# Performance work log

Measured on AMD Instinct MI355X. Metric: run time of the kernel, lower is better.

## Reference

```python
import jax, jax.numpy as jnp
import numpy as np

D = 128          # embedding dim
N_INIT = 100000  # number of initial (axiom) clauses
L = 64           # topological levels of derived clauses
M = 4096         # derived clauses per level
N_THAX = 2000    # distinct axiom-name (thax) embeddings
N_SINE = 32      # sine-level embeddings
N_RULES = 256    # distinct inference rules (each with its own 2-ary MLP)
N_TOT = N_INIT + L * M


def setup_inputs() -> dict:
    key = jax.random.key(0)
    ks = jax.random.split(key, 10)
    rng = np.random.default_rng(0)
    # parents of level-l nodes point to any node created strictly earlier
    parents = np.stack(
        [rng.integers(0, N_INIT + l * M, size=(M, 2)) for l in range(L)]
    ).astype(np.int32)  # [L, M, 2]
    return {
        "thax_table": jax.random.normal(ks[0], (N_THAX, D), jnp.float32) * 0.1,
        "sine_table": jax.random.normal(ks[1], (N_SINE, D), jnp.float32) * 0.1,
        "rule_W": jax.random.normal(ks[2], (N_RULES, 2 * D, D), jnp.float32) * (1.0 / np.sqrt(2 * D)),
        "rule_b": jax.random.normal(ks[3], (N_RULES, D), jnp.float32) * 0.01,
        "eval_w": jax.random.normal(ks[4], (D,), jnp.float32) * (1.0 / np.sqrt(D)),
        "eval_b": jax.random.normal(ks[5], (1,), jnp.float32) * 0.01,
        "pos_vals": jax.random.uniform(ks[6], (N_TOT,), jnp.float32, 0.01, 1.0),
        "neg_vals": jax.random.uniform(ks[7], (N_TOT,), jnp.float32, 0.01, 1.0),
        "init_thax": jax.random.randint(ks[8], (N_INIT,), 0, N_THAX, jnp.int32),
        "init_sine": jax.random.randint(ks[9], (N_INIT,), 0, N_SINE, jnp.int32),
        "parents": jnp.asarray(parents),
        "rules": jnp.asarray(rng.integers(0, N_RULES, size=(L, M)).astype(np.int32)),
    }


def reference(thax_table, sine_table, rule_W, rule_b, eval_w, eval_b,
              pos_vals, neg_vals, init_thax, init_sine, parents, rules):
    n_init = init_thax.shape[0]
    n_lvl, m = rules.shape
    d = thax_table.shape[1]

    # init nodes: embed = init_embeds[thax]() + sine_embedder(sine)
    init_emb = thax_table[init_thax] + sine_table[init_sine]  # [N_INIT, D]
    store0 = jnp.concatenate(
        [init_emb, jnp.zeros((n_lvl * m, d), init_emb.dtype)], axis=0)  # [N_TOT, D]

    # deriv nodes, level by level: gather 2 parents, per-rule MLP (cat -> Linear -> ReLU)
    def step(store, xs):
        lvl, par, rul = xs                       # par: [M,2] int, rul: [M] int
        pe = store[par].reshape(m, 2 * d)        # gather parent embeddings
        emb = jax.nn.relu(jnp.einsum('mi,mio->mo', pe, rule_W[rul]) + rule_b[rul])
        store = jax.lax.dynamic_update_slice(store, emb, (n_init + lvl * m, 0))
        return store, None

    store, _ = jax.lax.scan(step, store0, (jnp.arange(n_lvl), parents, rules))

    # eval_net + weighted BCEWithLogits (pos_weight = tot_neg / tot_pos)
    logits = store @ eval_w + eval_b[0]          # [N_TOT]
    tot = pos_vals + neg_vals
    y = pos_vals / tot
    pw = jnp.sum(neg_vals) / jnp.sum(pos_vals)
    per_node = pw * y * jax.nn.softplus(-logits) + (1.0 - y) * jax.nn.softplus(logits)
    loss = jnp.sum(tot * per_node).reshape(1)
    posOK = jnp.sum(jnp.where(logits >= 0.0, pos_vals, 0.0))
    negOK = jnp.sum(jnp.where(logits < 0.0, neg_vals, 0.0))
    return (loss, posOK, negOK)
```

## Files before the change

kernel.cpp:

```cpp
#include <hip/hip_runtime.h>

#define D      128
#define NINIT  100000
#define LVLS   64
#define M      4096
#define NRULES 256
#define NTOT   (NINIT + LVLS * M)
#define NBLK   256
#define NTHR   512
#define GRID_THREADS (NBLK * NTHR)

typedef __attribute__((ext_vector_type(8))) short short8;
typedef __attribute__((ext_vector_type(4))) float floatx4;

#define ST_OFF 256
#define SI_OFF (ST_OFF + (size_t)NTOT * D * 2)
#define RO_OFF (SI_OFF + (size_t)LVLS * M * 4)
#define FL_OFF (RO_OFF + (size_t)LVLS * (NRULES + 1) * 4)

__device__ __forceinline__ unsigned short f2bf(float x) {
  unsigned u = __float_as_uint(x);
  u += 0x7fffu + ((u >> 16) & 1u);
  return (unsigned short)(u >> 16);
}

__device__ __forceinline__ float softplusf(float x) {
  return fmaxf(x, 0.f) + log1pf(expf(-fabsf(x)));
}

__device__ __forceinline__ void st_sys(unsigned* p, unsigned v) {
  __hip_atomic_store(p, v, __ATOMIC_RELAXED, __HIP_MEMORY_SCOPE_SYSTEM);
}
__device__ __forceinline__ unsigned ld_sys(const unsigned* p) {
  return __hip_atomic_load(p, __ATOMIC_RELAXED, __HIP_MEMORY_SCOPE_SYSTEM);
}
__device__ __forceinline__ void wait_flag(const unsigned* f) {
  while (__builtin_expect(ld_sys(f) == 0u, 0))
    __builtin_amdgcn_s_sleep(2);
}

__device__ __forceinline__ void gbar(unsigned* bcnt, unsigned* bgen) {
  __syncthreads();
  if (threadIdx.x == 0) {
    unsigned g = __hip_atomic_load(bgen, __ATOMIC_RELAXED, __HIP_MEMORY_SCOPE_AGENT);
    unsigned v = __hip_atomic_fetch_add(bcnt, 1u, __ATOMIC_ACQ_REL, __HIP_MEMORY_SCOPE_AGENT);
    if (v == gridDim.x - 1) {
      __hip_atomic_store(bcnt, 0u, __ATOMIC_RELAXED, __HIP_MEMORY_SCOPE_AGENT);
      __hip_atomic_fetch_add(bgen, 1u, __ATOMIC_ACQ_REL, __HIP_MEMORY_SCOPE_AGENT);
    } else {
      while (__hip_atomic_load(bgen, __ATOMIC_RELAXED, __HIP_MEMORY_SCOPE_AGENT) == g)
        __builtin_amdgcn_s_sleep(1);
      __builtin_amdgcn_fence(__ATOMIC_ACQUIRE, "agent");
    }
  }
  __syncthreads();
}

__global__ __launch_bounds__(NTHR, 2) void fused_kernel(
    const float* __restrict__ thax_table, const float* __restrict__ sine_table,
    const float* __restrict__ rule_W, const float* __restrict__ rule_b,
    const float* __restrict__ eval_w, const float* __restrict__ eval_b,
    const float* __restrict__ pos, const float* __restrict__ neg,
    const int* __restrict__ init_thax, const int* __restrict__ init_sine,
    const int* __restrict__ parents,
    const int* __restrict__ rules,
    unsigned short* __restrict__ store, int* __restrict__ sorted_idx,
    int* __restrict__ rule_off, unsigned* __restrict__ flags,
    float* __restrict__ sums, unsigned* __restrict__ bvars,
    float* __restrict__ out) {
  __shared__ unsigned short pe[16 * 264];
  __shared__ unsigned short ot[16 * 136];
  __shared__ int s_sid[16];
  __shared__ int s_cnt[NRULES];
  __shared__ int s_base[NRULES + 1];
  __shared__ float racc[3];

  unsigned* bcnt = bvars;
  unsigned* bgen = bvars + 1;

  const int r = blockIdx.x;
  const int tid = threadIdx.x;
  const int wave = tid >> 6, lane = tid & 63;
  const int col = (wave << 4) + (lane & 15);
  const int snode = tid >> 5, seg = tid & 31;

  short8 bf[8];
  {
    const float* Wr = rule_W + (size_t)r * (2 * D * D);
    const int krow_base = (lane >> 4) * 8;
#pragma unroll
    for (int ks = 0; ks < 8; ++ks) {
      union { short8 s; unsigned short us[8]; } c;
#pragma unroll
      for (int j = 0; j < 8; ++j)
        c.us[j] = f2bf(Wr[(size_t)(ks * 32 + krow_base + j) * D + col]);
      bf[ks] = c.s;
    }
  }
  const float bias = rule_b[r * D + col];

  if (r < LVLS) {
    const int l = r;
    const int* rl = rules + (size_t)l * M;
    if (tid < NRULES) s_cnt[tid] = 0;
    __syncthreads();
    for (int m = tid; m < M; m += NTHR) atomicAdd(&s_cnt[rl[m]], 1);
    __syncthreads();
    if (tid == 0) {
      int run = 0;
      for (int q = 0; q < NRULES; ++q) { s_base[q] = run; run += s_cnt[q]; }
      s_base[NRULES] = run;
    }
    __syncthreads();
    if (tid < NRULES) {
      rule_off[(size_t)l * (NRULES + 1) + tid] = s_base[tid];
      s_cnt[tid] = s_base[tid];
    }
    if (tid == 0) rule_off[(size_t)l * (NRULES + 1) + NRULES] = M;
    __syncthreads();
    for (int m = tid; m < M; m += NTHR) {
      int p = atomicAdd(&s_cnt[rl[m]], 1);
      sorted_idx[(size_t)l * M + p] = m;
    }
  }

  for (int idx = r * NTHR + tid; idx < NINIT * 16; idx += GRID_THREADS) {
    int node = idx >> 4, sg = idx & 15;
    const float4* t = (const float4*)(thax_table + (size_t)init_thax[node] * D) + sg * 2;
    const float4* s = (const float4*)(sine_table + (size_t)init_sine[node] * D) + sg * 2;
    float4 a0 = t[0], a1 = t[1], b0 = s[0], b1 = s[1];
    float v[8] = {a0.x + b0.x, a0.y + b0.y, a0.z + b0.z, a0.w + b0.w,
                  a1.x + b1.x, a1.y + b1.y, a1.z + b1.z, a1.w + b1.w};
    uint4 pk;
    pk.x = (unsigned)f2bf(v[0]) | ((unsigned)f2bf(v[1]) << 16);
    pk.y = (unsigned)f2bf(v[2]) | ((unsigned)f2bf(v[3]) << 16);
    pk.z = (unsigned)f2bf(v[4]) | ((unsigned)f2bf(v[5]) << 16);
    pk.w = (unsigned)f2bf(v[6]) | ((unsigned)f2bf(v[7]) << 16);
    *(uint4*)(store + (size_t)node * D + sg * 8) = pk;
  }

  {
    float sp = 0.f, sn = 0.f;
    for (int i = r * NTHR + tid; i < NTOT; i += GRID_THREADS) {
      sp += pos[i];
      sn += neg[i];
    }
    for (int m = 32; m; m >>= 1) {
      sp += __shfl_xor(sp, m, 64);
      sn += __shfl_xor(sn, m, 64);
    }
    if (lane == 0) {
      atomicAdd(&sums[0], sp);
      atomicAdd(&sums[1], sn);
    }
  }

  gbar(bcnt, bgen);

  int off0, cnt, par0, sid0;
  {
    off0 = rule_off[r];
    cnt = rule_off[r + 1] - off0;
    int gj = cnt > 0 ? (snode < cnt ? snode : cnt - 1) : 0;
    int ii = off0 + gj; if (ii > M - 1) ii = M - 1;
    sid0 = sorted_idx[ii];
    par0 = parents[sid0 * 2 + (seg >> 4)];
  }

  for (int l = 0; l < LVLS; ++l) {
    const int* si_l = sorted_idx + (size_t)l * M;
    const int* par_l = parents + (size_t)l * M * 2;
    const int n_base = NINIT + l * M;
    const int fl_base = l * M;

    if (cnt > 0) {
      for (int t0 = 0; t0 < cnt; t0 += 16) {
        __syncthreads();
        {
          int par, sid;
          if (t0 == 0) {
            par = par0; sid = sid0;
          } else {
            int gj = t0 + snode; if (gj > cnt - 1) gj = cnt - 1;
            sid = si_l[off0 + gj];
            par = par_l[sid * 2 + (seg >> 4)];
          }
          if (seg == 0) s_sid[snode] = sid;
          if (par >= NINIT) wait_flag(flags + (par - NINIT));
          uint4 d = *(const uint4*)(store + (size_t)par * D + (seg & 15) * 8);
          *(uint4*)(pe + snode * 264 + seg * 8) = d;
        }
        __syncthreads();

        floatx4 acc = {0.f, 0.f, 0.f, 0.f};
#pragma unroll
        for (int ks = 0; ks < 8; ++ks) {
          short8 a = *(const short8*)(pe + (lane & 15) * 264 + ks * 32 + (lane >> 4) * 8);
          acc = __builtin_amdgcn_mfma_f32_16x16x32_bf16(a, bf[ks], acc, 0, 0, 0);
        }

#pragma unroll
        for (int reg = 0; reg < 4; ++reg) {
          int row = (lane >> 4) * 4 + reg;
          float v = acc[reg] + bias;
          ot[row * 136 + col] = f2bf(v > 0.f ? v : 0.f);
        }
        __syncthreads();

        {
          int q = tid;
#pragma unroll
          for (int rep = 0; rep < 2; ++rep, q += NTHR) {
            int node = q >> 6, off = q & 63;
            if (t0 + node < cnt) {
              unsigned val = *(const unsigned*)(ot + node * 136 + off * 2);
              unsigned* dst =
                  (unsigned*)(store + (size_t)(n_base + s_sid[node]) * D) + off;
              st_sys(dst, val);
            }
          }
        }
        __syncthreads();

        if (tid < 16 && t0 + tid < cnt)
          st_sys(flags + fl_base + s_sid[tid], 1u);
      }
    }

    if (l + 1 < LVLS) {
      const int* ro_n = rule_off + (size_t)(l + 1) * (NRULES + 1);
      int o = ro_n[r];
      int c = ro_n[r + 1] - o;
      int gj = c > 0 ? (snode < c ? snode : c - 1) : 0;
      int ii = o + gj; if (ii > M - 1) ii = M - 1;
      int sid = sorted_idx[(size_t)(l + 1) * M + ii];
      int pn = parents[((size_t)(l + 1) * M + sid) * 2 + (seg >> 4)];
      off0 = o; cnt = c; par0 = pn; sid0 = sid;
    }
  }

  gbar(bcnt, bgen);

  {
    float a_loss = 0.f, a_pos = 0.f, a_neg = 0.f;
    const float pw = sums[1] / sums[0];
    const float eb = eval_b[0];
    const float4* wv = (const float4*)eval_w;

    for (int node = r * NTHR + tid; node < NTOT; node += GRID_THREADS) {
      const uint4* v = (const uint4*)(store + (size_t)node * D);
      float dot = 0.f;
#pragma unroll
      for (int k = 0; k < 16; ++k) {
        uint4 u = v[k];
        float4 w0 = wv[k * 2], w1 = wv[k * 2 + 1];
        dot += __uint_as_float(u.x << 16) * w0.x +
               __uint_as_float(u.x & 0xffff0000u) * w0.y +
               __uint_as_float(u.y << 16) * w0.z +
               __uint_as_float(u.y & 0xffff0000u) * w0.w +
               __uint_as_float(u.z << 16) * w1.x +
               __uint_as_float(u.z & 0xffff0000u) * w1.y +
               __uint_as_float(u.w << 16) * w1.z +
               __uint_as_float(u.w & 0xffff0000u) * w1.w;
      }
      float logit = dot + eb;
      float p = pos[node], n = neg[node];
      float tot = p + n, y = p / tot;
      a_loss += tot * (pw * y * softplusf(-logit) + (1.f - y) * softplusf(logit));
      if (logit >= 0.f) a_pos += p; else a_neg += n;
    }

    for (int m = 32; m; m >>= 1) {
      a_loss += __shfl_xor(a_loss, m, 64);
      a_pos  += __shfl_xor(a_pos,  m, 64);
      a_neg  += __shfl_xor(a_neg,  m, 64);
    }
    if (tid == 0) { racc[0] = 0.f; racc[1] = 0.f; racc[2] = 0.f; }
    __syncthreads();
    if (lane == 0) {
      atomicAdd(&racc[0], a_loss);
      atomicAdd(&racc[1], a_pos);
      atomicAdd(&racc[2], a_neg);
    }
    __syncthreads();
    if (tid == 0) {
      atomicAdd(&out[0], racc[0]);
      atomicAdd(&out[1], racc[1]);
      atomicAdd(&out[2], racc[2]);
    }
  }
}

extern "C" void kernel_launch(void* const* d_in, const int* in_sizes, int n_in,
                              void* d_out, int out_size, void* d_ws, size_t ws_size,
                              hipStream_t stream) {
  const float* thax_table = (const float*)d_in[0];
  const float* sine_table = (const float*)d_in[1];
  const float* rule_W     = (const float*)d_in[2];
  const float* rule_b     = (const float*)d_in[3];
  const float* eval_w     = (const float*)d_in[4];
  const float* eval_b     = (const float*)d_in[5];
  const float* pos_vals   = (const float*)d_in[6];
  const float* neg_vals   = (const float*)d_in[7];
  const int*   init_thax  = (const int*)d_in[8];
  const int*   init_sine  = (const int*)d_in[9];
  const int*   parents    = (const int*)d_in[10];
  const int*   rules      = (const int*)d_in[11];

  float* out = (float*)d_out;
  char* ws = (char*)d_ws;
  float* sums = (float*)ws;
  unsigned* bvars = (unsigned*)(ws + 128);
  unsigned short* store = (unsigned short*)(ws + ST_OFF);
  int* sorted_idx = (int*)(ws + SI_OFF);
  int* rule_off   = (int*)(ws + RO_OFF);
  unsigned* flags = (unsigned*)(ws + FL_OFF);

  (void)hipMemsetAsync(d_out, 0, 3 * sizeof(float), stream);
  (void)hipMemsetAsync(d_ws, 0, 256, stream);
  (void)hipMemsetAsync(ws + FL_OFF, 0, (size_t)LVLS * M * 4, stream);

  void* args[] = {&thax_table, &sine_table, &rule_W, &rule_b, &eval_w, &eval_b,
                  &pos_vals, &neg_vals, &init_thax, &init_sine, &parents,
                  &rules, &store, &sorted_idx, &rule_off, &flags, &sums,
                  &bvars, &out};
  (void)hipLaunchCooperativeKernel((void*)fused_kernel, dim3(NBLK), dim3(NTHR),
                                   args, 0, stream);
}
```

Measured before the change: 480.2 us.

## Software-pipeline level tiles with a flattened cursor, prefetched parents and double-buffered LDS

```diff
diff --git a/kernel.cpp b/kernel.cpp
--- a/kernel.cpp
+++ b/kernel.cpp
@@ -35,11 +35,13 @@
   return __hip_atomic_load(p, __ATOMIC_RELAXED, __HIP_MEMORY_SCOPE_SYSTEM);
 }
 __device__ __forceinline__ void wait_flag(const unsigned* f) {
-  while (__builtin_expect(ld_sys(f) == 0u, 0))
+  int guard = 1 << 17;
+  while (__builtin_expect(ld_sys(f) == 0u, 0) && --guard)
     __builtin_amdgcn_s_sleep(2);
-}
-
-__device__ __forceinline__ void gbar(unsigned* bcnt, unsigned* bgen) {
+  asm volatile("" ::: "memory");
+}
+
+__device__ __forceinline__ void gbar_heavy(unsigned* bcnt, unsigned* bgen) {
   __syncthreads();
   if (threadIdx.x == 0) {
     unsigned g = __hip_atomic_load(bgen, __ATOMIC_RELAXED, __HIP_MEMORY_SCOPE_AGENT);
@@ -54,6 +56,35 @@
     }
   }
   __syncthreads();
+}
+
+__device__ __forceinline__ void gbar_light(unsigned* bcnt, unsigned* bgen) {
+  __syncthreads();
+  if (threadIdx.x == 0) {
+    unsigned g = ld_sys(bgen);
+    unsigned v = __hip_atomic_fetch_add(bcnt, 1u, __ATOMIC_RELAXED,
+                                        __HIP_MEMORY_SCOPE_SYSTEM);
+    if (v == gridDim.x - 1) {
+      st_sys(bcnt, 0u);
+      st_sys(bgen, g + 1u);
+    } else {
+      int guard = 1 << 22;
+      while (ld_sys(bgen) == g && --guard) __builtin_amdgcn_s_sleep(2);
+    }
+  }
+  __syncthreads();
+}
+
+__device__ __forceinline__ bool adv_cursor(int r, const int* __restrict__ ro,
+                                           int& l, int& t0, int& off, int& cnt) {
+  t0 += 16;
+  while (t0 >= cnt) {
+    if (++l >= LVLS) return false;
+    off = ro[l * (NRULES + 1) + r];
+    cnt = ro[l * (NRULES + 1) + r + 1] - off;
+    t0 = 0;
+  }
+  return true;
 }
 
 __global__ __launch_bounds__(NTHR, 2) void fused_kernel(
@@ -68,9 +99,9 @@
     int* __restrict__ rule_off, unsigned* __restrict__ flags,
     float* __restrict__ sums, unsigned* __restrict__ bvars,
     float* __restrict__ out) {
-  __shared__ unsigned short pe[16 * 264];
+  __shared__ unsigned short pe[2 * 16 * 264];
   __shared__ unsigned short ot[16 * 136];
-  __shared__ int s_sid[16];
+  __shared__ int s_sid[2][16];
   __shared__ int s_cnt[NRULES];
   __shared__ int s_base[NRULES + 1];
   __shared__ float racc[3];
@@ -83,6 +114,7 @@
   const int wave = tid >> 6, lane = tid & 63;
   const int col = (wave << 4) + (lane & 15);
   const int snode = tid >> 5, seg = tid & 31;
+  const int half = seg >> 4;
 
   short8 bf[8];
   {
@@ -155,91 +187,114 @@
     }
   }
 
-  gbar(bcnt, bgen);
-
-  int off0, cnt, par0, sid0;
-  {
-    off0 = rule_off[r];
-    cnt = rule_off[r + 1] - off0;
-    int gj = cnt > 0 ? (snode < cnt ? snode : cnt - 1) : 0;
-    int ii = off0 + gj; if (ii > M - 1) ii = M - 1;
-    sid0 = sorted_idx[ii];
-    par0 = parents[sid0 * 2 + (seg >> 4)];
-  }
-
-  for (int l = 0; l < LVLS; ++l) {
-    const int* si_l = sorted_idx + (size_t)l * M;
-    const int* par_l = parents + (size_t)l * M * 2;
-    const int n_base = NINIT + l * M;
-    const int fl_base = l * M;
-
-    if (cnt > 0) {
-      for (int t0 = 0; t0 < cnt; t0 += 16) {
-        __syncthreads();
-        {
-          int par, sid;
-          if (t0 == 0) {
-            par = par0; sid = sid0;
-          } else {
-            int gj = t0 + snode; if (gj > cnt - 1) gj = cnt - 1;
-            sid = si_l[off0 + gj];
-            par = par_l[sid * 2 + (seg >> 4)];
-          }
-          if (seg == 0) s_sid[snode] = sid;
-          if (par >= NINIT) wait_flag(flags + (par - NINIT));
-          uint4 d = *(const uint4*)(store + (size_t)par * D + (seg & 15) * 8);
-          *(uint4*)(pe + snode * 264 + seg * 8) = d;
-        }
-        __syncthreads();
-
-        floatx4 acc = {0.f, 0.f, 0.f, 0.f};
-#pragma unroll
-        for (int ks = 0; ks < 8; ++ks) {
-          short8 a = *(const short8*)(pe + (lane & 15) * 264 + ks * 32 + (lane >> 4) * 8);
-          acc = __builtin_amdgcn_mfma_f32_16x16x32_bf16(a, bf[ks], acc, 0, 0, 0);
-        }
-
-#pragma unroll
-        for (int reg = 0; reg < 4; ++reg) {
-          int row = (lane >> 4) * 4 + reg;
-          float v = acc[reg] + bias;
-          ot[row * 136 + col] = f2bf(v > 0.f ? v : 0.f);
-        }
-        __syncthreads();
-
-        {
-          int q = tid;
-#pragma unroll
-          for (int rep = 0; rep < 2; ++rep, q += NTHR) {
-            int node = q >> 6, off = q & 63;
-            if (t0 + node < cnt) {
-              unsigned val = *(const unsigned*)(ot + node * 136 + off * 2);
-              unsigned* dst =
-                  (unsigned*)(store + (size_t)(n_base + s_sid[node]) * D) + off;
-              st_sys(dst, val);
-            }
-          }
-        }
-        __syncthreads();
-
-        if (tid < 16 && t0 + tid < cnt)
-          st_sys(flags + fl_base + s_sid[tid], 1u);
+  gbar_heavy(bcnt, bgen);
+
+  int lL = -1, t0L = -16, offL = 0, cntL = 0;
+
+  bool validA = adv_cursor(r, rule_off, lL, t0L, offL, cntL);
+  int lA = lL, t0A = t0L, cntA = cntL;
+  int parA = 0; bool lateA = false; uint4 gA = {0, 0, 0, 0};
+  if (validA) {
+    int gj = t0A + snode; if (gj > cntA - 1) gj = cntA - 1;
+    int sid = sorted_idx[(size_t)lA * M + offL + gj];
+    parA = parents[((size_t)lA * M + sid) * 2 + half];
+    if (parA >= NINIT) wait_flag(flags + (parA - NINIT));
+    gA = *(const uint4*)(store + (size_t)parA * D + (seg & 15) * 8);
+    if (seg == 0) s_sid[0][snode] = sid;
+  }
+
+  bool validB = validA && adv_cursor(r, rule_off, lL, t0L, offL, cntL);
+  int lB = lL, t0B = t0L, cntB = cntL;
+  int parB = 0, sidB = 0; unsigned fB_val = 0u;
+  if (validB) {
+    int gj = t0B + snode; if (gj > cntB - 1) gj = cntB - 1;
+    sidB = sorted_idx[(size_t)lB * M + offL + gj];
+    parB = parents[((size_t)lB * M + sidB) * 2 + half];
+  }
+
+  bool validC = validB && adv_cursor(r, rule_off, lL, t0L, offL, cntL);
+  int lC = lL, t0C = t0L, cntC = cntL;
+  int parC = 0, sidC = 0;
+  if (validC) {
+    int gj = t0C + snode; if (gj > cntC - 1) gj = cntC - 1;
+    sidC = sorted_idx[(size_t)lC * M + offL + gj];
+    parC = parents[((size_t)lC * M + sidC) * 2 + half];
+  }
+
+  bool validD = validC && adv_cursor(r, rule_off, lL, t0L, offL, cntL);
+  int lD = lL, t0D = t0L, offD = offL, cntD = cntL;
+
+  int p = 0;
+  while (validA) {
+    if (lateA) {
+      wait_flag(flags + (parA - NINIT));
+      gA = *(const uint4*)(store + (size_t)parA * D + (seg & 15) * 8);
+    }
+    *(uint4*)(pe + p * (16 * 264) + snode * 264 + seg * 8) = gA;
+    __syncthreads();
+    if (validB && seg == 0) s_sid[p ^ 1][snode] = sidB;
+
+    floatx4 acc = {0.f, 0.f, 0.f, 0.f};
+#pragma unroll
+    for (int ks = 0; ks < 8; ++ks) {
+      short8 a = *(const short8*)(pe + p * (16 * 264) + (lane & 15) * 264 +
+                                  ks * 32 + (lane >> 4) * 8);
+      acc = __builtin_amdgcn_mfma_f32_16x16x32_bf16(a, bf[ks], acc, 0, 0, 0);
+    }
+#pragma unroll
+    for (int reg = 0; reg < 4; ++reg) {
+      int row = (lane >> 4) * 4 + reg;
+      float v = acc[reg] + bias;
+      ot[row * 136 + col] = f2bf(v > 0.f ? v : 0.f);
+    }
+    __syncthreads();
+
+    {
+      const int n_baseA = NINIT + lA * M;
+      int nsid0 = s_sid[p][wave], nsid1 = s_sid[p][wave + 8];
+      bool in0 = (t0A + wave) < cntA, in1 = (t0A + wave + 8) < cntA;
+      if (in0)
+        st_sys((unsigned*)(store + (size_t)(n_baseA + nsid0) * D) + lane,
+               *(const unsigned*)(ot + wave * 136 + lane * 2));
+      if (in1)
+        st_sys((unsigned*)(store + (size_t)(n_baseA + nsid1) * D) + lane,
+               *(const unsigned*)(ot + (wave + 8) * 136 + lane * 2));
+      asm volatile("s_waitcnt vmcnt(0)" ::: "memory");
+      if (lane == 0) {
+        if (in0) st_sys(flags + lA * M + nsid0, 1u);
+        if (in1) st_sys(flags + lA * M + nsid1, 1u);
       }
-    }
-
-    if (l + 1 < LVLS) {
-      const int* ro_n = rule_off + (size_t)(l + 1) * (NRULES + 1);
-      int o = ro_n[r];
-      int c = ro_n[r + 1] - o;
-      int gj = c > 0 ? (snode < c ? snode : c - 1) : 0;
-      int ii = o + gj; if (ii > M - 1) ii = M - 1;
-      int sid = sorted_idx[(size_t)(l + 1) * M + ii];
-      int pn = parents[((size_t)(l + 1) * M + sid) * 2 + (seg >> 4)];
-      off0 = o; cnt = c; par0 = pn; sid0 = sid;
-    }
-  }
-
-  gbar(bcnt, bgen);
+      asm volatile("" ::: "memory");
+    }
+
+    unsigned fC_val = 1u;
+    if (validC && parC >= NINIT) fC_val = ld_sys(flags + (parC - NINIT));
+
+    bool lateB = false; uint4 gB = {0, 0, 0, 0};
+    if (validB) {
+      if (parB >= NINIT && fB_val == 0u) lateB = true;
+      else gB = *(const uint4*)(store + (size_t)parB * D + (seg & 15) * 8);
+    }
+
+    int parD = 0, sidD = 0;
+    if (validD) {
+      int gj = t0D + snode; if (gj > cntD - 1) gj = cntD - 1;
+      sidD = sorted_idx[(size_t)lD * M + offD + gj];
+      parD = parents[((size_t)lD * M + sidD) * 2 + half];
+    }
+
+    gA = gB; lateA = lateB; parA = parB;
+    lA = lB; t0A = t0B; cntA = cntB; validA = validB;
+    parB = parC; sidB = sidC; fB_val = fC_val;
+    lB = lC; t0B = t0C; cntB = cntC; validB = validC;
+    parC = parD; sidC = sidD;
+    lC = lD; t0C = t0D; cntC = cntD; validC = validD;
+    validD = validC && adv_cursor(r, rule_off, lL, t0L, offL, cntL);
+    lD = lL; t0D = t0L; offD = offL; cntD = cntL;
+    p ^= 1;
+  }
+
+  gbar_light(bcnt, bgen);
 
   {
     float a_loss = 0.f, a_pos = 0.f, a_neg = 0.f;
@@ -264,10 +319,10 @@
                __uint_as_float(u.w & 0xffff0000u) * w1.w;
       }
       float logit = dot + eb;
-      float p = pos[node], n = neg[node];
-      float tot = p + n, y = p / tot;
+      float pp = pos[node], nn = neg[node];
+      float tot = pp + nn, y = pp / tot;
       a_loss += tot * (pw * y * softplusf(-logit) + (1.f - y) * softplusf(logit));
-      if (logit >= 0.f) a_pos += p; else a_neg += n;
+      if (logit >= 0.f) a_pos += pp; else a_neg += nn;
     }
 
     for (int m = 32; m; m >>= 1) {
```

After: 430.5 us. 1.12x faster.
